# Kernel optimization log

Measured on AMD Instinct MI355X. Metric: run time of the kernel, lower is better.

The kernel has to match this reference:

```python
import jax, jax.numpy as jnp
import numpy as np

NUM_HEADS = 16
ALPHA = 1.0          # attention_logits_alpha
SOFTCAP = 50.0       # logit_softcapping


def setup_inputs() -> dict:
    key = jax.random.key(0)
    ks = jax.random.split(key, 7)
    B, S, E = 2, 2048, 2048
    mk = lambda k, shape, sc=1.0: jax.random.normal(k, shape, dtype=jnp.float32) * sc
    return {
        "q": mk(ks[0], (B, S, E)),
        "k": mk(ks[1], (B, S, E)),
        "v": mk(ks[2], (B, S, E)),
        # nn.Linear weights are [out, in]; xavier-ish scale 1/sqrt(E)
        "Wq": mk(ks[3], (E, E), E ** -0.5),
        "Wk": mk(ks[4], (E, E), E ** -0.5),
        "Wv": mk(ks[5], (E, E), E ** -0.5),
        "Wo": mk(ks[6], (E, E), E ** -0.5),
    }


def reference(q, k, v, Wq, Wk, Wv, Wo):
    B, S, E = q.shape
    H = NUM_HEADS
    D = E // H  # head_dim = 128

    def split_heads(x):  # [B,S,E] -> [B,H,S,D]
        return x.reshape(B, S, H, D).transpose(0, 2, 1, 3)

    qh = split_heads(q @ Wq.T)  # q_projection_scale = 1.0
    kh = split_heads(k @ Wk.T)
    vh = split_heads(v @ Wv.T)

    # scaled_dot_product: scale q by 1/sqrt(head_dim)
    qh = qh * (D ** -0.5)
    logits = ALPHA * jnp.einsum("bhqd,bhkd->bhqk", qh, kh)
    # logit softcapping: cap * tanh(logits / cap)
    logits = SOFTCAP * jnp.tanh(logits / SOFTCAP)
    # fp32 softmax (softmax_dtype_fp32=True)
    probs = jax.nn.softmax(logits.astype(jnp.float32), axis=-1).astype(qh.dtype)
    # dropout rate 0.0 -> identity
    ctx = jnp.einsum("bhqk,bhkd->bhqd", probs, vh)
    ctx = ctx.transpose(0, 2, 1, 3).reshape(B, S, E)
    return ctx @ Wo.T  # output_projection_scale = 1.0
```

## Files before the change

### kernel.cpp

```cpp
#include <hip/hip_runtime.h>
#include <hip/hip_bf16.h>
#include <stdint.h>


typedef __attribute__((ext_vector_type(8))) short s16x8;
typedef __attribute__((ext_vector_type(4))) float f32x4;

typedef const __attribute__((address_space(1))) char* gcptr;
typedef __attribute__((address_space(3))) char* lcptr;

#define MFMA_BF16(a, b, c) __builtin_amdgcn_mfma_f32_16x16x32_bf16((a), (b), (c), 0, 0, 0)

__device__ __forceinline__ short f2bf(float f) {
  union { float f; unsigned u; } x; x.f = f;
  unsigned r = (x.u + 0x7fffu + ((x.u >> 16) & 1u)) >> 16;
  return (short)r;
}

__device__ __forceinline__ void gload16(const void* g, void* lds) {
  __builtin_amdgcn_global_load_lds((gcptr)g, (lcptr)lds, 16, 0, 0);
}

constexpr int GK = 2048;
constexpr int SL = 2048, EMB = 2048, HD = 128;

__global__ void cvt_all(const float* __restrict__ q, const float* __restrict__ k,
                        const float* __restrict__ v, const float* __restrict__ wq,
                        const float* __restrict__ wk, const float* __restrict__ wv,
                        const float* __restrict__ wo, short* __restrict__ dst) {
  const int N8A = 1 << 20, N8W = 1 << 19;
  const int total = 3 * N8A + 4 * N8W;
  int i = blockIdx.x * blockDim.x + threadIdx.x;
  int stride = gridDim.x * blockDim.x;
  for (; i < total; i += stride) {
    const float* src;
    size_t loc;
    if (i < 3 * N8A) {
      int sel = i >> 20;
      loc = (size_t)(i & (N8A - 1));
      src = sel == 0 ? q : (sel == 1 ? k : v);
    } else {
      int w = i - 3 * N8A;
      int sel = w >> 19;
      loc = (size_t)(w & (N8W - 1));
      src = sel == 0 ? wq : (sel == 1 ? wk : (sel == 2 ? wv : wo));
    }
    f32x4 a = *reinterpret_cast<const f32x4*>(src + loc * 8);
    f32x4 b = *reinterpret_cast<const f32x4*>(src + loc * 8 + 4);
    s16x8 w8;
#pragma unroll
    for (int j = 0; j < 4; ++j) { w8[j] = f2bf(a[j]); w8[4 + j] = f2bf(b[j]); }
    *reinterpret_cast<s16x8*>(dst + (size_t)i * 8) = w8;
  }
}

__global__ __launch_bounds__(256, 2)
void gemm_qkv(const short* __restrict__ a0, const short* __restrict__ a1,
              const short* __restrict__ w0, const short* __restrict__ w1,
              const short* __restrict__ w2, const short* __restrict__ a2,
              short* __restrict__ o0, short* __restrict__ o1,
              short* __restrict__ o2) {
  __shared__ __align__(16) short As[128 * 64];
  __shared__ __align__(16) short Bs[128 * 64];
  const int z = blockIdx.z;
  const short* A = z == 0 ? a0 : (z == 1 ? a1 : w2);
  const short* B = z == 0 ? w0 : (z == 1 ? w1 : a2);
  short* C = z == 0 ? o0 : (z == 1 ? o1 : o2);

  const int d = blockIdx.x + (blockIdx.y << 4);
  const int tile = ((d & 7) << 6) | (d >> 3);
  const int bm = z == 2 ? (tile & 15) : (tile >> 4);
  const int bn = z == 2 ? (tile >> 4) : (tile & 15);
  const int gn = z == 2 ? 4096 : 2048;

  const int tid = threadIdx.x;
  const int lane = tid & 63;
  const int wid = tid >> 6;
  const int wr = wid >> 1, wc = wid & 1;
  const int g = lane >> 4, r = lane & 15;

  const f32x4 fz = {0.f, 0.f, 0.f, 0.f};
  f32x4 acc[4][4];
#pragma unroll
  for (int m = 0; m < 4; ++m)
#pragma unroll
    for (int n = 0; n < 4; ++n) acc[m][n] = fz;

  const short* Ab = A + (size_t)bm * 128 * GK;
  const short* Bb = B + (size_t)bn * 128 * GK;

  for (int kt = 0; kt < GK; kt += 64) {
#pragma unroll
    for (int i = 0; i < 4; ++i) {
      int c = i * 256 + tid;
      int row = c >> 3, c8 = c & 7;
      gload16(Ab + (size_t)row * GK + kt + c8 * 8, As + c * 8);
      gload16(Bb + (size_t)row * GK + kt + c8 * 8, Bs + c * 8);
    }
    __syncthreads();
#pragma unroll
    for (int kk = 0; kk < 2; ++kk) {
      s16x8 af[4], bf[4];
#pragma unroll
      for (int m = 0; m < 4; ++m)
        af[m] = *reinterpret_cast<const s16x8*>(As + (wr * 64 + m * 16 + r) * 64 + kk * 32 + g * 8);
#pragma unroll
      for (int n = 0; n < 4; ++n)
        bf[n] = *reinterpret_cast<const s16x8*>(Bs + (wc * 64 + n * 16 + r) * 64 + kk * 32 + g * 8);
#pragma unroll
      for (int m = 0; m < 4; ++m)
#pragma unroll
        for (int n = 0; n < 4; ++n) acc[m][n] = MFMA_BF16(af[m], bf[n], acc[m][n]);
    }
    __syncthreads();
  }

#pragma unroll
  for (int m = 0; m < 4; ++m)
#pragma unroll
    for (int j = 0; j < 4; ++j) {
      int crow = bm * 128 + wr * 64 + m * 16 + g * 4 + j;
      size_t off = (size_t)crow * gn + bn * 128 + wc * 64 + r;
#pragma unroll
      for (int n = 0; n < 4; ++n) C[off + n * 16] = f2bf(acc[m][n][j]);
    }
}

__global__ __launch_bounds__(256, 2)
void gemm_out(const short* __restrict__ A, const short* __restrict__ B,
              float* __restrict__ C) {
  __shared__ __align__(16) short As[128 * 64];
  __shared__ __align__(16) short Bs[128 * 64];
  const int d = blockIdx.x + (blockIdx.y << 4);
  const int tile = ((d & 7) << 6) | (d >> 3);
  const int bm = tile >> 4, bn = tile & 15;

  const int tid = threadIdx.x;
  const int lane = tid & 63;
  const int wid = tid >> 6;
  const int wr = wid >> 1, wc = wid & 1;
  const int g = lane >> 4, r = lane & 15;

  const f32x4 fz = {0.f, 0.f, 0.f, 0.f};
  f32x4 acc[4][4];
#pragma unroll
  for (int m = 0; m < 4; ++m)
#pragma unroll
    for (int n = 0; n < 4; ++n) acc[m][n] = fz;

  const short* Ab = A + (size_t)bm * 128 * GK;
  const short* Bb = B + (size_t)bn * 128 * GK;

  for (int kt = 0; kt < GK; kt += 64) {
#pragma unroll
    for (int i = 0; i < 4; ++i) {
      int c = i * 256 + tid;
      int row = c >> 3, c8 = c & 7;
      gload16(Ab + (size_t)row * GK + kt + c8 * 8, As + c * 8);
      gload16(Bb + (size_t)row * GK + kt + c8 * 8, Bs + c * 8);
    }
    __syncthreads();
#pragma unroll
    for (int kk = 0; kk < 2; ++kk) {
      s16x8 af[4], bf[4];
#pragma unroll
      for (int m = 0; m < 4; ++m)
        af[m] = *reinterpret_cast<const s16x8*>(As + (wr * 64 + m * 16 + r) * 64 + kk * 32 + g * 8);
#pragma unroll
      for (int n = 0; n < 4; ++n)
        bf[n] = *reinterpret_cast<const s16x8*>(Bs + (wc * 64 + n * 16 + r) * 64 + kk * 32 + g * 8);
#pragma unroll
      for (int m = 0; m < 4; ++m)
#pragma unroll
        for (int n = 0; n < 4; ++n) acc[m][n] = MFMA_BF16(af[m], bf[n], acc[m][n]);
    }
    __syncthreads();
  }

#pragma unroll
  for (int m = 0; m < 4; ++m)
#pragma unroll
    for (int j = 0; j < 4; ++j) {
      int crow = bm * 128 + wr * 64 + m * 16 + g * 4 + j;
      size_t off = (size_t)crow * 2048 + bn * 128 + wc * 64 + r;
#pragma unroll
      for (int n = 0; n < 4; ++n) C[off + n * 16] = acc[m][n][j];
    }
}

__global__ __launch_bounds__(256, 2)
void attn(const short* __restrict__ Q, const short* __restrict__ K,
          const short* __restrict__ VT, short* __restrict__ O) {
  __shared__ __align__(16) short Ks[64 * 136];
  __shared__ __align__(16) short Vt[128 * 72];
  __shared__ __align__(16) short Ps[4][2][16 * 72];

  const int tid = threadIdx.x;
  const int lane = tid & 63;
  const int wid = tid >> 6;
  const int g = lane >> 4, r = lane & 15;

  const int dflat = blockIdx.x + (blockIdx.y << 4);
  const int cflat = ((dflat & 7) << 6) + (dflat >> 3);
  const int qb = cflat & 15;
  const int bh = cflat >> 4;
  const int b = bh >> 4, h = bh & 15;
  const size_t base = (size_t)b * SL * EMB + (size_t)h * HD;
  const size_t vbase = (size_t)h * HD * 4096 + (size_t)b * SL;

  const int q0 = qb * 128 + wid * 32;
  s16x8 qf[2][4];
#pragma unroll
  for (int s = 0; s < 2; ++s)
#pragma unroll
    for (int kk = 0; kk < 4; ++kk)
      qf[s][kk] = *reinterpret_cast<const s16x8*>(
          Q + base + (size_t)(q0 + s * 16 + r) * EMB + kk * 32 + g * 8);

  const f32x4 fz = {0.f, 0.f, 0.f, 0.f};
  float l_run[2][4];
  f32x4 acc_o[2][8];
#pragma unroll
  for (int s = 0; s < 2; ++s) {
#pragma unroll
    for (int i = 0; i < 4; ++i) l_run[s][i] = 0.f;
#pragma unroll
    for (int i = 0; i < 8; ++i) acc_o[s][i] = fz;
  }

  const float SCALE = 0.08838834764831845f;
  const float C50I = 0.02f;
  const float CA = -1.f / 3.f, CB = 2.f / 15.f;

  const int rk = tid >> 4, ck = tid & 15;
  const int rv = tid >> 3, cv = tid & 7;
  const int cvx = cv ^ (rv & 7);
  s16x8 kreg[4], vreg[4];
#pragma unroll
  for (int i = 0; i < 4; ++i) {
    kreg[i] = *reinterpret_cast<const s16x8*>(K + base + (size_t)(rk + i * 16) * EMB + ck * 8);
    vreg[i] = *reinterpret_cast<const s16x8*>(VT + vbase + (size_t)(rv + i * 32) * 4096 + cv * 8);
  }

  for (int t = 0; t < SL / 64; ++t) {
    __syncthreads();
#pragma unroll
    for (int i = 0; i < 4; ++i) {
      *reinterpret_cast<s16x8*>(&Ks[(rk + i * 16) * 136 + ck * 8]) = kreg[i];
      *reinterpret_cast<s16x8*>(&Vt[(rv + i * 32) * 72 + (cvx << 3)]) = vreg[i];
    }
    __syncthreads();

    if (t + 1 < SL / 64) {
      const int kv1 = (t + 1) * 64;
#pragma unroll
      for (int i = 0; i < 4; ++i) {
        kreg[i] = *reinterpret_cast<const s16x8*>(K + base + (size_t)(kv1 + rk + i * 16) * EMB + ck * 8);
        vreg[i] = *reinterpret_cast<const s16x8*>(VT + vbase + (size_t)(rv + i * 32) * 4096 + kv1 + cv * 8);
      }
    }

    f32x4 sv[2][4];
    __builtin_amdgcn_s_setprio(1);
#pragma unroll
    for (int kn = 0; kn < 4; ++kn) {
      sv[0][kn] = fz; sv[1][kn] = fz;
#pragma unroll
      for (int kk = 0; kk < 4; ++kk) {
        s16x8 kf = *reinterpret_cast<const s16x8*>(&Ks[(kn * 16 + r) * 136 + kk * 32 + g * 8]);
        sv[0][kn] = MFMA_BF16(qf[0][kk], kf, sv[0][kn]);
        sv[1][kn] = MFMA_BF16(qf[1][kk], kf, sv[1][kn]);
      }
    }
    __builtin_amdgcn_s_setprio(0);

#pragma unroll
    for (int s = 0; s < 2; ++s)
#pragma unroll
      for (int kn = 0; kn < 4; ++kn)
#pragma unroll
        for (int reg = 0; reg < 4; ++reg) {
          float z = sv[s][kn][reg] * SCALE;
          float x = z * C50I;
          float x2 = x * x;
          float poly = __builtin_fmaf(x2, __builtin_fmaf(x2, CB, CA), 1.f);
          float cap = fminf(z * poly, 50.f);
          float pe = __expf(cap - 50.f);
          l_run[s][reg] += pe;
          sv[s][kn][reg] = pe;
        }

#pragma unroll
    for (int s = 0; s < 2; ++s)
#pragma unroll
      for (int kn = 0; kn < 4; ++kn)
#pragma unroll
        for (int reg = 0; reg < 4; ++reg)
          Ps[wid][s][(g * 4 + reg) * 72 + kn * 16 + r] = f2bf(sv[s][kn][reg]);

    __builtin_amdgcn_s_setprio(1);
#pragma unroll
    for (int c = 0; c < 2; ++c) {
      s16x8 pa0 = *reinterpret_cast<const s16x8*>(&Ps[wid][0][r * 72 + c * 32 + g * 8]);
      s16x8 pa1 = *reinterpret_cast<const s16x8*>(&Ps[wid][1][r * 72 + c * 32 + g * 8]);
#pragma unroll
      for (int dn = 0; dn < 8; ++dn) {
        int d = dn * 16 + r;
        int pc = ((c * 4 + g) ^ (r & 7));
        s16x8 vf = *reinterpret_cast<const s16x8*>(&Vt[d * 72 + (pc << 3)]);
        acc_o[0][dn] = MFMA_BF16(pa0, vf, acc_o[0][dn]);
        acc_o[1][dn] = MFMA_BF16(pa1, vf, acc_o[1][dn]);
      }
    }
    __builtin_amdgcn_s_setprio(0);
  }

#pragma unroll
  for (int s = 0; s < 2; ++s) {
#pragma unroll
    for (int reg = 0; reg < 4; ++reg) {
#pragma unroll
      for (int off = 1; off < 16; off <<= 1)
        l_run[s][reg] += __shfl_xor(l_run[s][reg], off);
      l_run[s][reg] = 1.f / l_run[s][reg];
    }
#pragma unroll
    for (int dn = 0; dn < 8; ++dn)
#pragma unroll
      for (int reg = 0; reg < 4; ++reg) {
        int row = q0 + s * 16 + g * 4 + reg;
        O[base + (size_t)row * EMB + dn * 16 + r] = f2bf(acc_o[s][dn][reg] * l_run[s][reg]);
      }
  }
}

__global__ void fill_f32(float* p, int n, float val) {
  int i = blockIdx.x * blockDim.x + threadIdx.x;
  if (i < n) p[i] = val;
}

extern "C" void kernel_launch(void* const* d_in, const int* in_sizes, int n_in,
                              void* d_out, int out_size, void* d_ws, size_t ws_size,
                              hipStream_t stream) {
  const float* q  = (const float*)d_in[0];
  const float* k  = (const float*)d_in[1];
  const float* v  = (const float*)d_in[2];
  const float* wq = (const float*)d_in[3];
  const float* wk = (const float*)d_in[4];
  const float* wv = (const float*)d_in[5];
  const float* wo = (const float*)d_in[6];
  float* out = (float*)d_out;

  bool ok = (n_in == 7) && out_size == 8388608;
  for (int i = 0; i < 3 && ok; ++i) ok = (in_sizes[i] == 8388608);
  for (int i = 3; i < 7 && ok; ++i) ok = (in_sizes[i] == 4194304);
  if (!ok) {
    fill_f32<<<(out_size + 255) / 256, 256, 0, stream>>>(out, out_size, 150.f);
    return;
  }

  const size_t NA = 8388608;
  const size_t NW = 4194304;
  const size_t need = (3 * NA + 4 * NW + 4 * NA) * sizeof(short);
  if (ws_size < need) {
    fill_f32<<<(out_size + 255) / 256, 256, 0, stream>>>(out, out_size, 128.f);
    return;
  }

  short* bq  = (short*)d_ws;
  short* bk  = bq + NA;
  short* bv  = bk + NA;
  short* bwq = bv + NA;
  short* bwk = bwq + NW;
  short* bwv = bwk + NW;
  short* bwo = bwv + NW;
  short* Qp  = bwo + NW;
  short* Kp  = Qp + NA;
  short* VpT = Kp + NA;
  short* Cx  = VpT + NA;

  dim3 blk(256);
  dim3 g3(16, 32, 3);
  dim3 gg(16, 32);
  dim3 ga(16, 32);

  cvt_all<<<2048, 256, 0, stream>>>(q, k, v, wq, wk, wv, wo, bq);
  gemm_qkv<<<g3, blk, 0, stream>>>(bq, bk, bwq, bwk, bwv, bv, Qp, Kp, VpT);
  attn<<<ga, blk, 0, stream>>>(Qp, Kp, VpT, Cx);
  gemm_out<<<gg, blk, 0, stream>>>(Cx, bwo, out);
}
```

Before: 340.1 us.

## Rewrite QKV projection GEMM with 256x256 tiles and multi-stage async LDS pipeline

Replaces the 128x128, 256-thread QKV GEMM with a 512-thread kernel computing 256x256 tiles. Each K step is 32 wide and uses a 4-slot LDS ring buffer, with loads issued three steps ahead and gated by vmcnt waits. A XOR swizzle avoids LDS bank conflicts, and MFMA priority is raised with s_setprio. The aim is to hide global load latency and raise arithmetic intensity, at the cost of 128 KB of LDS per block (one block per CU) and higher register pressure.

```diff
diff --git a/kernel.cpp b/kernel.cpp
--- a/kernel.cpp
+++ b/kernel.cpp
@@ -54,75 +54,106 @@
   }
 }
 
-__global__ __launch_bounds__(256, 2)
-void gemm_qkv(const short* __restrict__ a0, const short* __restrict__ a1,
-              const short* __restrict__ w0, const short* __restrict__ w1,
-              const short* __restrict__ w2, const short* __restrict__ a2,
-              short* __restrict__ o0, short* __restrict__ o1,
-              short* __restrict__ o2) {
-  __shared__ __align__(16) short As[128 * 64];
-  __shared__ __align__(16) short Bs[128 * 64];
+__global__ __launch_bounds__(512, 1)
+void gemm8_qkv(const short* __restrict__ a0, const short* __restrict__ a1,
+               const short* __restrict__ w0, const short* __restrict__ w1,
+               const short* __restrict__ w2, const short* __restrict__ a2,
+               short* __restrict__ o0, short* __restrict__ o1,
+               short* __restrict__ o2) {
+  __shared__ __align__(16) short Lds[4 * 16384];
+
   const int z = blockIdx.z;
   const short* A = z == 0 ? a0 : (z == 1 ? a1 : w2);
   const short* B = z == 0 ? w0 : (z == 1 ? w1 : a2);
   short* C = z == 0 ? o0 : (z == 1 ? o1 : o2);
-
-  const int d = blockIdx.x + (blockIdx.y << 4);
-  const int tile = ((d & 7) << 6) | (d >> 3);
-  const int bm = z == 2 ? (tile & 15) : (tile >> 4);
-  const int bn = z == 2 ? (tile >> 4) : (tile & 15);
   const int gn = z == 2 ? 4096 : 2048;
+
+  const int j = blockIdx.x + (blockIdx.y << 3);
+  int bm, bn;
+  if (z == 2) { bm = j & 7; bn = j >> 3; }
+  else        { bm = ((j & 7) << 1) + ((j >> 3) & 1); bn = j >> 4; }
 
   const int tid = threadIdx.x;
   const int lane = tid & 63;
   const int wid = tid >> 6;
-  const int wr = wid >> 1, wc = wid & 1;
+  const int wm = wid >> 2, wn = wid & 3;
   const int g = lane >> 4, r = lane & 15;
+  const int pg = g ^ ((r >> 1) & 3);
+
+  const size_t Abase = (size_t)bm * 256 * GK;
+  const size_t Bbase = (size_t)bn * 256 * GK;
 
   const f32x4 fz = {0.f, 0.f, 0.f, 0.f};
-  f32x4 acc[4][4];
-#pragma unroll
-  for (int m = 0; m < 4; ++m)
+  f32x4 acc[8][4];
+#pragma unroll
+  for (int m = 0; m < 8; ++m)
 #pragma unroll
     for (int n = 0; n < 4; ++n) acc[m][n] = fz;
 
-  const short* Ab = A + (size_t)bm * 128 * GK;
-  const short* Bb = B + (size_t)bn * 128 * GK;
-
-  for (int kt = 0; kt < GK; kt += 64) {
-#pragma unroll
-    for (int i = 0; i < 4; ++i) {
-      int c = i * 256 + tid;
-      int row = c >> 3, c8 = c & 7;
-      gload16(Ab + (size_t)row * GK + kt + c8 * 8, As + c * 8);
-      gload16(Bb + (size_t)row * GK + kt + c8 * 8, Bs + c * 8);
-    }
-    __syncthreads();
-#pragma unroll
-    for (int kk = 0; kk < 2; ++kk) {
-      s16x8 af[4], bf[4];
-#pragma unroll
-      for (int m = 0; m < 4; ++m)
-        af[m] = *reinterpret_cast<const s16x8*>(As + (wr * 64 + m * 16 + r) * 64 + kk * 32 + g * 8);
-#pragma unroll
-      for (int n = 0; n < 4; ++n)
-        bf[n] = *reinterpret_cast<const s16x8*>(Bs + (wc * 64 + n * 16 + r) * 64 + kk * 32 + g * 8);
-#pragma unroll
-      for (int m = 0; m < 4; ++m)
-#pragma unroll
-        for (int n = 0; n < 4; ++n) acc[m][n] = MFMA_BF16(af[m], bf[n], acc[m][n]);
-    }
-    __syncthreads();
-  }
-
-#pragma unroll
-  for (int m = 0; m < 4; ++m)
-#pragma unroll
-    for (int j = 0; j < 4; ++j) {
-      int crow = bm * 128 + wr * 64 + m * 16 + g * 4 + j;
-      size_t off = (size_t)crow * gn + bn * 128 + wc * 64 + r;
-#pragma unroll
-      for (int n = 0; n < 4; ++n) C[off + n * 16] = f2bf(acc[m][n][j]);
+  auto issueHalf = [&](int n) {
+    const int reg = (n & 3) * 16384;
+    const int k0 = (n << 5) & (GK - 1);
+#pragma unroll
+    for (int i = 0; i < 2; ++i) {
+      int c = tid + i * 512;
+      int row = c >> 2;
+      int lg = (c & 3) ^ ((c >> 3) & 3);
+      gload16(A + Abase + (size_t)row * GK + k0 + lg * 8, Lds + reg + c * 8);
+    }
+#pragma unroll
+    for (int i = 0; i < 2; ++i) {
+      int c = tid + i * 512;
+      int row = c >> 2;
+      int lg = (c & 3) ^ ((c >> 3) & 3);
+      gload16(B + Bbase + (size_t)row * GK + k0 + lg * 8, Lds + reg + 8192 + c * 8);
+    }
+  };
+
+  issueHalf(0);
+  issueHalf(1);
+  issueHalf(2);
+
+  for (int t2 = 0; t2 < 16; ++t2) {
+#pragma unroll
+    for (int p = 0; p < 4; ++p) {
+      const int n = t2 * 4 + p;
+      issueHalf(n + 3);
+      asm volatile("s_waitcnt vmcnt(12)" ::: "memory");
+      asm volatile("s_barrier" ::: "memory");
+
+      const int areg = p * 16384;
+      s16x8 af[8], bf[4];
+#pragma unroll
+      for (int m = 0; m < 8; ++m)
+        af[m] = *reinterpret_cast<const s16x8*>(
+            Lds + areg + ((wm * 128 + m * 16 + r) << 5) + pg * 8);
+#pragma unroll
+      for (int nf = 0; nf < 4; ++nf)
+        bf[nf] = *reinterpret_cast<const s16x8*>(
+            Lds + areg + 8192 + ((wn * 64 + nf * 16 + r) << 5) + pg * 8);
+
+      __builtin_amdgcn_s_setprio(1);
+#pragma unroll
+      for (int m = 0; m < 8; ++m)
+#pragma unroll
+        for (int nf = 0; nf < 4; ++nf)
+          acc[m][nf] = MFMA_BF16(af[m], bf[nf], acc[m][nf]);
+      __builtin_amdgcn_s_setprio(0);
+
+      asm volatile("s_waitcnt lgkmcnt(0)" ::: "memory");
+      asm volatile("s_barrier" ::: "memory");
+    }
+  }
+  asm volatile("s_waitcnt vmcnt(0)" ::: "memory");
+
+#pragma unroll
+  for (int m = 0; m < 8; ++m)
+#pragma unroll
+    for (int jj = 0; jj < 4; ++jj) {
+      int crow = bm * 256 + wm * 128 + m * 16 + g * 4 + jj;
+      size_t off = (size_t)crow * gn + bn * 256 + wn * 64 + r;
+#pragma unroll
+      for (int nf = 0; nf < 4; ++nf) C[off + nf * 16] = f2bf(acc[m][nf][jj]);
     }
 }
 
@@ -180,11 +211,11 @@
 #pragma unroll
   for (int m = 0; m < 4; ++m)
 #pragma unroll
-    for (int j = 0; j < 4; ++j) {
-      int crow = bm * 128 + wr * 64 + m * 16 + g * 4 + j;
+    for (int jj = 0; jj < 4; ++jj) {
+      int crow = bm * 128 + wr * 64 + m * 16 + g * 4 + jj;
       size_t off = (size_t)crow * 2048 + bn * 128 + wc * 64 + r;
 #pragma unroll
-      for (int n = 0; n < 4; ++n) C[off + n * 16] = acc[m][n][j];
+      for (int n = 0; n < 4; ++n) C[off + n * 16] = acc[m][n][jj];
     }
 }
 
@@ -379,13 +410,12 @@
   short* VpT = Kp + NA;
   short* Cx  = VpT + NA;
 
-  dim3 blk(256);
-  dim3 g3(16, 32, 3);
+  dim3 g8(8, 16, 3);
   dim3 gg(16, 32);
   dim3 ga(16, 32);
 
   cvt_all<<<2048, 256, 0, stream>>>(q, k, v, wq, wk, wv, wo, bq);
-  gemm_qkv<<<g3, blk, 0, stream>>>(bq, bk, bwq, bwk, bwv, bv, Qp, Kp, VpT);
-  attn<<<ga, blk, 0, stream>>>(Qp, Kp, VpT, Cx);
-  gemm_out<<<gg, blk, 0, stream>>>(Cx, bwo, out);
-}
+  gemm8_qkv<<<g8, dim3(512), 0, stream>>>(bq, bk, bwq, bwk, bwv, bv, Qp, Kp, VpT);
+  attn<<<ga, dim3(256), 0, stream>>>(Qp, Kp, VpT, Cx);
+  gemm_out<<<gg, dim3(256), 0, stream>>>(Cx, bwo, out);
+}
```

Result: faster. 326.1 us (median of 2 runs) (-4.1%).
